# Performance work log

Measured on AMD Instinct MI355X. Metric: run time of the kernel, lower is better.

The kernel has to match this reference:

```python
import jax, jax.numpy as jnp
import numpy as np

S = 8192
D = 512

def setup_inputs() -> dict:
    key = jax.random.key(0)
    k1, k2, k3, k4 = jax.random.split(key, 4)
    token_encodings = jax.random.normal(k1, (S, D), dtype=jnp.float32)
    # causal mask: True where attention is disallowed (strictly upper triangular)
    mask = jnp.triu(jnp.ones((S, S), dtype=bool), k=1)
    W_q = jax.random.normal(k2, (D, D), dtype=jnp.float32) * (1.0 / np.sqrt(D))
    W_k = jax.random.normal(k3, (D, D), dtype=jnp.float32) * (1.0 / np.sqrt(D))
    W_v = jax.random.normal(k4, (D, D), dtype=jnp.float32) * (1.0 / np.sqrt(D))
    return {"token_encodings": token_encodings, "mask": mask, "W_q": W_q, "W_k": W_k, "W_v": W_v}

def reference(token_encodings, mask, W_q, W_k, W_v):
    # nn.Linear(bias=False): y = x @ W^T
    q = token_encodings @ W_q.T  # [S, D]
    k = token_encodings @ W_k.T  # [S, D]
    v = token_encodings @ W_v.T  # [S, D]
    scale = jnp.asarray(k.shape[1], dtype=q.dtype) ** 0.5
    sims = (q @ k.T) / scale  # [S, S]
    sims = jnp.where(mask, jnp.asarray(-1e9, dtype=sims.dtype), sims)
    attn = jax.nn.softmax(sims, axis=1)
    return attn @ v  # [S, D]
```

## Files before the change

### kernel.cpp

```cpp
#include <hip/hip_runtime.h>
#include <stdint.h>

typedef _Float16 f16;
typedef _Float16 f16x8 __attribute__((ext_vector_type(8)));
typedef _Float16 f16x4 __attribute__((ext_vector_type(4)));
typedef float f32x4 __attribute__((ext_vector_type(4)));

#define S_TOK 8192
#define DDIM  512
#define L2E   1.44269504088896340736f
#define QSCALE 0.04419417382415922f
#define NSLOT 320
#define GTOT  8320

__device__ __forceinline__ void gload_lds16(const void* g, void* l) {
  __builtin_amdgcn_global_load_lds((const __attribute__((address_space(1))) void*)g,
                                   (__attribute__((address_space(3))) void*)l, 16, 0, 0);
}

template <int C>
__device__ __forceinline__ float fdpp(float x) {
  return __builtin_bit_cast(float,
      __builtin_amdgcn_update_dpp(0, __builtin_bit_cast(int, x), C, 0xF, 0xF, true));
}
__device__ __forceinline__ float rowmax16(float x) {
  x = fmaxf(x, fdpp<0xB1>(x));
  x = fmaxf(x, fdpp<0x4E>(x));
  x = fmaxf(x, fdpp<0x141>(x));
  x = fmaxf(x, fdpp<0x140>(x));
  return x;
}
__device__ __forceinline__ float rowsum16(float x) {
  x += fdpp<0xB1>(x);
  x += fdpp<0x4E>(x);
  x += fdpp<0x141>(x);
  x += fdpp<0x140>(x);
  return x;
}

__global__ __launch_bounds__(256) void k_convert(
    const float* __restrict__ X, const float* __restrict__ Wq,
    const float* __restrict__ Wk, const float* __restrict__ Wv,
    f16* __restrict__ Xh, f16* __restrict__ Wh, int* __restrict__ tp) {
  const int SD = S_TOK * DDIM;
  const int DD = DDIM * DDIM;
  int gi = blockIdx.x * 256 + threadIdx.x;
  if (gi < NSLOT) tp[gi] = -1;
  int i4 = gi * 4;
  if (i4 < SD) {
    f32x4 v = *(const f32x4*)(X + i4);
    f16x4 h = {(f16)v[0], (f16)v[1], (f16)v[2], (f16)v[3]};
    *(f16x4*)(Xh + i4) = h;
  } else {
    int j = i4 - SD;
    int mat = j >> 18;
    const float* src = (mat == 0) ? Wq : (mat == 1 ? Wk : Wv);
    f32x4 v = *(const f32x4*)(src + (j & (DD - 1)));
    f16x4 h = {(f16)v[0], (f16)v[1], (f16)v[2], (f16)v[3]};
    *(f16x4*)(Wh + j) = h;
  }
}

__global__ __launch_bounds__(256) void k_proj(
    const f16* __restrict__ Xh, const f16* __restrict__ Wh,
    f16* __restrict__ Qh, f16* __restrict__ KB, f16* __restrict__ VB) {
  __shared__ __align__(16) char Al[128 * 128];
  __shared__ __align__(16) char Bl[128 * 128];
  const int tid = threadIdx.x;
  const int w = tid >> 6, lane = tid & 63;
  const int m0 = blockIdx.x * 128;
  const int n0 = blockIdx.y * 128;
  const int wr = (w >> 1) * 64;
  const int wc = (w & 1) * 64;

  f32x4 acc[4][4];
#pragma unroll
  for (int i = 0; i < 4; ++i)
#pragma unroll
    for (int j = 0; j < 4; ++j) acc[i][j] = (f32x4){0.f, 0.f, 0.f, 0.f};

  const char* Xb = (const char*)Xh;
  const char* Wb = (const char*)Wh;

  for (int kb = 0; kb < DDIM; kb += 64) {
    __syncthreads();
#pragma unroll
    for (int i = 0; i < 4; ++i) {
      int ch = w * 4 + i;
      int srow = lane >> 3;
      int scol = ((lane & 7) * 16) ^ (srow << 4);
      gload_lds16(Xb + (size_t)(m0 + ch * 8 + srow) * 1024 + kb * 2 + scol, Al + ch * 1024);
      gload_lds16(Wb + (size_t)(n0 + ch * 8 + srow) * 1024 + kb * 2 + scol, Bl + ch * 1024);
    }
    __syncthreads();
#pragma unroll
    for (int ks = 0; ks < 2; ++ks) {
      f16x8 a[4], b[4];
#pragma unroll
      for (int mf = 0; mf < 4; ++mf) {
        int row = wr + mf * 16 + (lane & 15);
        int col = (ks * 64 + ((lane >> 4) * 16)) ^ ((row & 7) << 4);
        a[mf] = *(const f16x8*)(Al + row * 128 + col);
      }
#pragma unroll
      for (int nf = 0; nf < 4; ++nf) {
        int row = wc + nf * 16 + (lane & 15);
        int col = (ks * 64 + ((lane >> 4) * 16)) ^ ((row & 7) << 4);
        b[nf] = *(const f16x8*)(Bl + row * 128 + col);
      }
#pragma unroll
      for (int mf = 0; mf < 4; ++mf)
#pragma unroll
        for (int nf = 0; nf < 4; ++nf)
          acc[mf][nf] = __builtin_amdgcn_mfma_f32_16x16x32_f16(a[mf], b[nf], acc[mf][nf], 0, 0, 0);
    }
  }
  int mat = n0 >> 9;
  int nbase = n0 & 511;
  if (mat == 2) {
#pragma unroll
    for (int mf = 0; mf < 4; ++mf) {
      int R0 = m0 + wr + mf * 16 + (lane >> 4) * 4;
      int K = R0 >> 5;
      int lhi = ((R0 >> 3) & 3) * 16;
      int j0 = R0 & 7;
#pragma unroll
      for (int nf = 0; nf < 4; ++nf) {
        int col = nbase + wc + nf * 16 + (lane & 15);
        f16x4 h = {(f16)acc[mf][nf][0], (f16)acc[mf][nf][1],
                   (f16)acc[mf][nf][2], (f16)acc[mf][nf][3]};
        *(f16x4*)((char*)VB + (size_t)(K * 32 + (col >> 4)) * 1024 +
                  (lhi + (col & 15)) * 16 + j0 * 2) = h;
      }
    }
  } else if (mat == 1) {
#pragma unroll
    for (int mf = 0; mf < 4; ++mf)
#pragma unroll
      for (int nf = 0; nf < 4; ++nf)
#pragma unroll
        for (int r = 0; r < 4; ++r) {
          int token = m0 + wr + mf * 16 + (lane >> 4) * 4 + r;
          int d = nbase + wc + nf * 16 + (lane & 15);
          size_t byte = (size_t)(token >> 5) * 32768 + (size_t)((token >> 4) & 1) * 16384
                      + (size_t)(d >> 5) * 1024
                      + (token & 15) * 16 + ((d >> 3) & 3) * 256 + (d & 7) * 2;
          *(f16*)((char*)KB + byte) = (f16)acc[mf][nf][r];
        }
  } else {
    float scale = QSCALE;
#pragma unroll
    for (int mf = 0; mf < 4; ++mf)
#pragma unroll
      for (int nf = 0; nf < 4; ++nf)
#pragma unroll
        for (int r = 0; r < 4; ++r) {
          int row = m0 + wr + mf * 16 + (lane >> 4) * 4 + r;
          int col = nbase + wc + nf * 16 + (lane & 15);
          Qh[(size_t)row * DDIM + col] = (f16)(acc[mf][nf][r] * scale);
        }
  }
}

__global__ __launch_bounds__(512, 2) void k_flash(
    const f16* __restrict__ Qh, const f16* __restrict__ KBg,
    const f16* __restrict__ VBg, f16* __restrict__ Opart,
    float* __restrict__ Mpart, float* __restrict__ Lpart,
    int* __restrict__ TilePart) {
  __shared__ __align__(16) char Kl[2][32768];
  __shared__ __align__(16) char Vl[2][32768];
  __shared__ __align__(16) char Pl[8][2][1152];

  const int tid = threadIdx.x;
  const int w = tid >> 6, lane = tid & 63;
  const int l15 = lane & 15, l4 = lane >> 4;

  int bid = blockIdx.x;
  int b = (bid & 7) * 32 + (bid >> 3);
  int g  = (GTOT * b) >> 8;
  int g1 = (GTOT * (b + 1)) >> 8;
  int t = 0;
  while (2 * (t + 1) * (t + 2) <= g) ++t;

  const char* Kb = (const char*)KBg;
  const char* Vb = (const char*)VBg;

#define STAGEKV(KB_, BI) do {                                                  \
    const char* ks_ = Kb + (size_t)((KB_) >> 5) * 32768;                       \
    _Pragma("unroll")                                                          \
    for (int i_ = 0; i_ < 4; ++i_) {                                           \
      int ch_ = w * 4 + i_;                                                    \
      gload_lds16(ks_ + ch_ * 1024 + lane * 16, Kl[BI] + ch_ * 1024);          \
    }                                                                          \
    const char* vs_ = Vb + (size_t)(KB_) * 1024;                               \
    _Pragma("unroll")                                                          \
    for (int i_ = 0; i_ < 4; ++i_) {                                           \
      int ch_ = w * 4 + i_;                                                    \
      gload_lds16(vs_ + ch_ * 1024 + lane * 16, Vl[BI] + ch_ * 1024);          \
    } } while (0)

#define SOFTMAX(KB_, Pdst) do {                                                \
    float p0[4], p1[4], mx[4];                                                 \
    int qrb = q0 + w * 16 + l4 * 4;                                            \
    int kc = (KB_) + l15;                                                      \
    _Pragma("unroll")                                                          \
    for (int r = 0; r < 4; ++r) {                                              \
      int qr = qrb + r;                                                        \
      float x0 = (kc      <= qr) ? s0[r] : -3.0e38f;                           \
      float x1 = (kc + 16 <= qr) ? s1[r] : -3.0e38f;                           \
      p0[r] = x0; p1[r] = x1;                                                  \
      mx[r] = rowmax16(fmaxf(x0, x1));                                         \
    }                                                                          \
    bool need = (mx[0] > mreg[0] + 8.f) || (mx[1] > mreg[1] + 8.f) ||          \
                (mx[2] > mreg[2] + 8.f) || (mx[3] > mreg[3] + 8.f);            \
    if (__any(need)) {                                                         \
      float alpha[4];                                                          \
      _Pragma("unroll")                                                        \
      for (int r = 0; r < 4; ++r) {                                            \
        float mn = fmaxf(mreg[r], mx[r]);                                      \
        alpha[r] = exp2f((mreg[r] - mn) * L2E);                                \
        lreg[r] *= alpha[r];                                                   \
        mreg[r] = mn;                                                          \
      }                                                                        \
      _Pragma("unroll")                                                        \
      for (int nf = 0; nf < 32; ++nf) {                                        \
        acc[nf][0] *= alpha[0];                                                \
        acc[nf][1] *= alpha[1];                                                \
        acc[nf][2] *= alpha[2];                                                \
        acc[nf][3] *= alpha[3];                                                \
      }                                                                        \
    }                                                                          \
    _Pragma("unroll")                                                          \
    for (int r = 0; r < 4; ++r) {                                              \
      int qr = qrb + r;                                                        \
      p0[r] = (kc      <= qr) ? exp2f((p0[r] - mreg[r]) * L2E) : 0.f;          \
      p1[r] = (kc + 16 <= qr) ? exp2f((p1[r] - mreg[r]) * L2E) : 0.f;          \
    }                                                                          \
    _Pragma("unroll")                                                          \
    for (int r = 0; r < 4; ++r) {                                              \
      int row = l4 * 4 + r;                                                    \
      *(f16*)((Pdst) + row * 72 + l15 * 2)      = (f16)p0[r];                  \
      *(f16*)((Pdst) + row * 72 + 32 + l15 * 2) = (f16)p1[r];                  \
    }                                                                          \
    _Pragma("unroll")                                                          \
    for (int r = 0; r < 4; ++r)                                                \
      lreg[r] += rowsum16(p0[r] + p1[r]);                                      \
  } while (0)

#define QKT(BUF) do {                                                          \
    s0 = (f32x4){0.f, 0.f, 0.f, 0.f};                                          \
    s1 = (f32x4){0.f, 0.f, 0.f, 0.f};                                          \
    const char* kp_ = (BUF) + lane * 16;                                       \
    __builtin_amdgcn_s_setprio(1);                                             \
    _Pragma("unroll")                                                          \
    for (int ks = 0; ks < 16; ++ks) {                                          \
      f16x8 kf0 = *(const f16x8*)(kp_ + ks * 1024);                            \
      s0 = __builtin_amdgcn_mfma_f32_16x16x32_f16(qf[ks], kf0, s0, 0, 0, 0);   \
      f16x8 kf1 = *(const f16x8*)(kp_ + 16384 + ks * 1024);                    \
      s1 = __builtin_amdgcn_mfma_f32_16x16x32_f16(qf[ks], kf1, s1, 0, 0, 0);   \
    }                                                                          \
    __builtin_amdgcn_s_setprio(0); } while (0)

#define PV(BI) do {                                                            \
    const char* VlB_ = Vl[BI] + lane * 16;                                     \
    const char* Pp_ = Pw + (BI) * 1152;                                        \
    f16x8 pa_ = *(const f16x8*)(Pp_ + l15 * 72 + l4 * 16);                     \
    __builtin_amdgcn_s_setprio(1);                                             \
    _Pragma("unroll")                                                          \
    for (int nf = 0; nf < 32; ++nf) {                                          \
      f16x8 vb_ = *(const f16x8*)(VlB_ + nf * 1024);                           \
      acc[nf] = __builtin_amdgcn_mfma_f32_16x16x32_f16(pa_, vb_, acc[nf], 0, 0, 0); \
    }                                                                          \
    __builtin_amdgcn_s_setprio(0); } while (0)

  char* Pw = (char*)Pl + (size_t)w * 2304;

  while (g < g1) {
    int Ct  = 2 * t * (t + 1);
    int Ct1 = 2 * (t + 1) * (t + 2);
    int gend = min(g1, Ct1);
    int n = gend - g;
    int kb0 = (g - Ct) * 32;
    int q0 = t * 128;
    int slot = b + t;

    f16x8 qf[16];
    {
      const f16* qp = Qh + (size_t)(q0 + w * 16 + l15) * DDIM + l4 * 8;
#pragma unroll
      for (int ks = 0; ks < 16; ++ks) qf[ks] = *(const f16x8*)(qp + ks * 32);
    }
    f32x4 acc[32];
#pragma unroll
    for (int i = 0; i < 32; ++i) acc[i] = (f32x4){0.f, 0.f, 0.f, 0.f};
    float mreg[4], lreg[4];
#pragma unroll
    for (int r = 0; r < 4; ++r) { mreg[r] = -3.0e38f; lreg[r] = 0.f; }
    f32x4 s0, s1;

    STAGEKV(kb0, 0);
    asm volatile("s_waitcnt vmcnt(0)" ::: "memory");
    __builtin_amdgcn_s_barrier();
    if (n > 1) STAGEKV(kb0 + 32, 1);
    QKT(Kl[0]);
    SOFTMAX(kb0, Pw);

    for (int it = 1; it < n; ++it) {
      PV((it - 1) & 1);
      asm volatile("s_waitcnt vmcnt(0)" ::: "memory");
      __builtin_amdgcn_s_barrier();
      if (it + 1 < n) STAGEKV(kb0 + (it + 1) * 32, (it + 1) & 1);
      QKT(Kl[it & 1]);
      SOFTMAX(kb0 + it * 32, Pw + (it & 1) * 1152);
    }

    PV((n - 1) & 1);
    __builtin_amdgcn_s_barrier();

    {
      float inv[4];
#pragma unroll
      for (int r = 0; r < 4; ++r) inv[r] = (lreg[r] > 0.f) ? 1.f / lreg[r] : 0.f;
      f16* op = Opart + (size_t)slot * (128 * 512);
      int rowb = w * 16 + l4 * 4;
#pragma unroll
      for (int nf = 0; nf < 32; ++nf) {
        int col = nf * 16 + l15;
#pragma unroll
        for (int r = 0; r < 4; ++r)
          op[(size_t)(rowb + r) * 512 + col] = (f16)(acc[nf][r] * inv[r]);
      }
      if (l15 == 0) {
#pragma unroll
        for (int r = 0; r < 4; ++r) {
          Mpart[slot * 128 + rowb + r] = mreg[r];
          Lpart[slot * 128 + rowb + r] = lreg[r];
        }
      }
      if (tid == 0) TilePart[slot] = t;
    }
    g = gend;
    ++t;
  }
#undef STAGEKV
#undef SOFTMAX
#undef QKT
#undef PV
}

__global__ __launch_bounds__(256) void k_reduce(
    const f16* __restrict__ Opart, const float* __restrict__ Mpart,
    const float* __restrict__ Lpart, const int* __restrict__ TilePart,
    float* __restrict__ out) {
  __shared__ int tp[NSLOT];
  __shared__ int sl[16];
  __shared__ int scnt;
  int tid = threadIdx.x;
  int t = blockIdx.x >> 2, rg = blockIdx.x & 3;
  for (int s = tid; s < NSLOT; s += 256) tp[s] = TilePart[s];
  __syncthreads();
  if (tid == 0) {
    int c = 0;
    for (int s = 0; s < NSLOT; ++s)
      if (tp[s] == t && c < 16) sl[c++] = s;
    scnt = c;
  }
  __syncthreads();
  int cnt = scnt;
  int rowIn = rg * 32 + (tid >> 3);
  int row = t * 128 + rowIn;
  int col0 = (tid & 7) * 64;

  float M = -3.0e38f;
  for (int i = 0; i < cnt; ++i) M = fmaxf(M, Mpart[sl[i] * 128 + rowIn]);
  float a[64];
#pragma unroll
  for (int j = 0; j < 64; ++j) a[j] = 0.f;
  float denom = 0.f;
  for (int i = 0; i < cnt; ++i) {
    int s = sl[i];
    float m = Mpart[s * 128 + rowIn];
    float l = Lpart[s * 128 + rowIn];
    float wgt = exp2f((m - M) * L2E) * l;
    denom += wgt;
    const f16* op = Opart + (size_t)s * 65536 + rowIn * 512 + col0;
#pragma unroll
    for (int v = 0; v < 8; ++v) {
      f16x8 x = *(const f16x8*)(op + v * 8);
#pragma unroll
      for (int j = 0; j < 8; ++j) a[v * 8 + j] += wgt * (float)x[j];
    }
  }
  float inv = (denom > 0.f) ? 1.f / denom : 0.f;
  float* o = out + (size_t)row * 512 + col0;
#pragma unroll
  for (int j = 0; j < 64; ++j) o[j] = a[j] * inv;
}

extern "C" void kernel_launch(void* const* d_in, const int* in_sizes, int n_in,
                              void* d_out, int out_size, void* d_ws, size_t ws_size,
                              hipStream_t stream) {
  const float* X  = (const float*)d_in[0];
  const float* Wq = (const float*)d_in[2];
  const float* Wk = (const float*)d_in[3];
  const float* Wv = (const float*)d_in[4];
  float* out = (float*)d_out;

  char* ws = (char*)d_ws;
  f16*   Opart = (f16*)(ws);
  float* Mpart = (float*)(ws + (40u << 20));
  float* Lpart = (float*)(ws + (41u << 20));
  int*   TileP = (int*)(ws + (42u << 20));
  f16* Qh = (f16*)(ws + (43u << 20));
  f16* KB = (f16*)(ws + (51u << 20));
  f16* VB = (f16*)(ws + (59u << 20));
  f16* Xh = (f16*)(ws + (67u << 20));
  f16* Wh = (f16*)(ws + (75u << 20));

  k_convert<<<4864, 256, 0, stream>>>(X, Wq, Wk, Wv, Xh, Wh, TileP);
  dim3 gp(64, 12);
  k_proj<<<gp, 256, 0, stream>>>(Xh, Wh, Qh, KB, VB);
  k_flash<<<256, 512, 0, stream>>>(Qh, KB, VB, Opart, Mpart, Lpart, TileP);
  k_reduce<<<256, 256, 0, stream>>>(Opart, Mpart, Lpart, TileP, out);
}
```

Before: 213.1 us.

## Repartition PV so each wave owns a 64-column output slice via shared P

```diff
diff --git a/kernel.cpp b/kernel.cpp
--- a/kernel.cpp
+++ b/kernel.cpp
@@ -5,6 +5,7 @@
 typedef _Float16 f16x8 __attribute__((ext_vector_type(8)));
 typedef _Float16 f16x4 __attribute__((ext_vector_type(4)));
 typedef float f32x4 __attribute__((ext_vector_type(4)));
+typedef int   i32x4 __attribute__((ext_vector_type(4)));
 
 #define S_TOK 8192
 #define DDIM  512
@@ -169,7 +170,10 @@
     int* __restrict__ TilePart) {
   __shared__ __align__(16) char Kl[2][32768];
   __shared__ __align__(16) char Vl[2][32768];
-  __shared__ __align__(16) char Pl[8][2][1152];
+  __shared__ __align__(16) char Pl[2][9216];
+  __shared__ __align__(16) float Alph[128];
+  __shared__ __align__(16) float Ll[128];
+  __shared__ __align__(16) int Fl[8];
 
   const int tid = threadIdx.x;
   const int w = tid >> 6, lane = tid & 63;
@@ -200,7 +204,7 @@
     } } while (0)
 
 #define SOFTMAX(KB_, Pdst) do {                                                \
-    float p0[4], p1[4], mx[4];                                                 \
+    float p0[4], p1[4], mx[4], alpha[4];                                       \
     int qrb = q0 + w * 16 + l4 * 4;                                            \
     int kc = (KB_) + l15;                                                      \
     _Pragma("unroll")                                                          \
@@ -213,8 +217,8 @@
     }                                                                          \
     bool need = (mx[0] > mreg[0] + 8.f) || (mx[1] > mreg[1] + 8.f) ||          \
                 (mx[2] > mreg[2] + 8.f) || (mx[3] > mreg[3] + 8.f);            \
-    if (__any(need)) {                                                         \
-      float alpha[4];                                                          \
+    need = __any(need);                                                        \
+    if (need) {                                                                \
       _Pragma("unroll")                                                        \
       for (int r = 0; r < 4; ++r) {                                            \
         float mn = fmaxf(mreg[r], mx[r]);                                      \
@@ -222,14 +226,15 @@
         lreg[r] *= alpha[r];                                                   \
         mreg[r] = mn;                                                          \
       }                                                                        \
+    } else {                                                                   \
       _Pragma("unroll")                                                        \
-      for (int nf = 0; nf < 32; ++nf) {                                        \
-        acc[nf][0] *= alpha[0];                                                \
-        acc[nf][1] *= alpha[1];                                                \
-        acc[nf][2] *= alpha[2];                                                \
-        acc[nf][3] *= alpha[3];                                                \
-      }                                                                        \
-    }                                                                          \
+      for (int r = 0; r < 4; ++r) alpha[r] = 1.0f;                             \
+    }                                                                          \
+    if (l15 == 0) {                                                            \
+      _Pragma("unroll")                                                        \
+      for (int r = 0; r < 4; ++r) Alph[w * 16 + l4 * 4 + r] = alpha[r];        \
+    }                                                                          \
+    if (lane == 0) Fl[w] = need ? 1 : 0;                                       \
     _Pragma("unroll")                                                          \
     for (int r = 0; r < 4; ++r) {                                              \
       int qr = qrb + r;                                                        \
@@ -238,7 +243,7 @@
     }                                                                          \
     _Pragma("unroll")                                                          \
     for (int r = 0; r < 4; ++r) {                                              \
-      int row = l4 * 4 + r;                                                    \
+      int row = w * 16 + l4 * 4 + r;                                           \
       *(f16*)((Pdst) + row * 72 + l15 * 2)      = (f16)p0[r];                  \
       *(f16*)((Pdst) + row * 72 + 32 + l15 * 2) = (f16)p1[r];                  \
     }                                                                          \
@@ -262,18 +267,36 @@
     __builtin_amdgcn_s_setprio(0); } while (0)
 
 #define PV(BI) do {                                                            \
-    const char* VlB_ = Vl[BI] + lane * 16;                                     \
-    const char* Pp_ = Pw + (BI) * 1152;                                        \
-    f16x8 pa_ = *(const f16x8*)(Pp_ + l15 * 72 + l4 * 16);                     \
+    i32x4 f0_ = *(const i32x4*)(Fl);                                           \
+    i32x4 f1_ = *(const i32x4*)(Fl + 4);                                       \
+    int fl_ = f0_[0] | f0_[1] | f0_[2] | f0_[3] | f1_[0] | f1_[1] | f1_[2] | f1_[3]; \
+    if (fl_) {                                                                 \
+      _Pragma("unroll")                                                        \
+      for (int rf = 0; rf < 8; ++rf) {                                         \
+        f32x4 av_ = *(const f32x4*)(Alph + rf * 16 + l4 * 4);                  \
+        _Pragma("unroll")                                                      \
+        for (int cf = 0; cf < 4; ++cf) {                                       \
+          acc[rf * 4 + cf][0] *= av_[0];                                       \
+          acc[rf * 4 + cf][1] *= av_[1];                                       \
+          acc[rf * 4 + cf][2] *= av_[2];                                       \
+          acc[rf * 4 + cf][3] *= av_[3];                                       \
+        }                                                                      \
+      }                                                                        \
+    }                                                                          \
+    f16x8 vbf_[4];                                                             \
+    _Pragma("unroll")                                                          \
+    for (int cf = 0; cf < 4; ++cf)                                             \
+      vbf_[cf] = *(const f16x8*)(Vl[BI] + (w * 4 + cf) * 1024 + lane * 16);    \
+    const char* pb_ = Pl[BI] + l15 * 72 + l4 * 16;                             \
     __builtin_amdgcn_s_setprio(1);                                             \
     _Pragma("unroll")                                                          \
-    for (int nf = 0; nf < 32; ++nf) {                                          \
-      f16x8 vb_ = *(const f16x8*)(VlB_ + nf * 1024);                           \
-      acc[nf] = __builtin_amdgcn_mfma_f32_16x16x32_f16(pa_, vb_, acc[nf], 0, 0, 0); \
+    for (int rf = 0; rf < 8; ++rf) {                                           \
+      f16x8 pa_ = *(const f16x8*)(pb_ + rf * 1152);                            \
+      _Pragma("unroll")                                                        \
+      for (int cf = 0; cf < 4; ++cf)                                           \
+        acc[rf * 4 + cf] = __builtin_amdgcn_mfma_f32_16x16x32_f16(pa_, vbf_[cf], acc[rf * 4 + cf], 0, 0, 0); \
     }                                                                          \
     __builtin_amdgcn_s_setprio(0); } while (0)
-
-  char* Pw = (char*)Pl + (size_t)w * 2304;
 
   while (g < g1) {
     int Ct  = 2 * t * (t + 1);
@@ -301,44 +324,54 @@
     STAGEKV(kb0, 0);
     asm volatile("s_waitcnt vmcnt(0)" ::: "memory");
     __builtin_amdgcn_s_barrier();
-    if (n > 1) STAGEKV(kb0 + 32, 1);
-    QKT(Kl[0]);
-    SOFTMAX(kb0, Pw);
-
-    for (int it = 1; it < n; ++it) {
-      PV((it - 1) & 1);
+
+    for (int it = 0; it < n; ++it) {
+      int cur = it & 1;
+      if (it + 1 < n) STAGEKV(kb0 + (it + 1) * 32, cur ^ 1);
+      QKT(Kl[cur]);
+      SOFTMAX(kb0 + it * 32, Pl[cur]);
+      asm volatile("s_waitcnt lgkmcnt(0)" ::: "memory");
+      __builtin_amdgcn_s_barrier();
+      PV(cur);
       asm volatile("s_waitcnt vmcnt(0)" ::: "memory");
       __builtin_amdgcn_s_barrier();
-      if (it + 1 < n) STAGEKV(kb0 + (it + 1) * 32, (it + 1) & 1);
-      QKT(Kl[it & 1]);
-      SOFTMAX(kb0 + it * 32, Pw + (it & 1) * 1152);
-    }
-
-    PV((n - 1) & 1);
+    }
+
+    if (l15 == 0) {
+#pragma unroll
+      for (int r = 0; r < 4; ++r) Ll[w * 16 + l4 * 4 + r] = lreg[r];
+    }
+    asm volatile("s_waitcnt lgkmcnt(0)" ::: "memory");
     __builtin_amdgcn_s_barrier();
-
     {
-      float inv[4];
-#pragma unroll
-      for (int r = 0; r < 4; ++r) inv[r] = (lreg[r] > 0.f) ? 1.f / lreg[r] : 0.f;
       f16* op = Opart + (size_t)slot * (128 * 512);
-      int rowb = w * 16 + l4 * 4;
-#pragma unroll
-      for (int nf = 0; nf < 32; ++nf) {
-        int col = nf * 16 + l15;
-#pragma unroll
-        for (int r = 0; r < 4; ++r)
-          op[(size_t)(rowb + r) * 512 + col] = (f16)(acc[nf][r] * inv[r]);
+#pragma unroll
+      for (int rf = 0; rf < 8; ++rf) {
+        f32x4 lv = *(const f32x4*)(Ll + rf * 16 + l4 * 4);
+        f32x4 inv;
+#pragma unroll
+        for (int r = 0; r < 4; ++r) inv[r] = (lv[r] > 0.f) ? 1.f / lv[r] : 0.f;
+#pragma unroll
+        for (int cf = 0; cf < 4; ++cf) {
+          int col = w * 64 + cf * 16 + l15;
+#pragma unroll
+          for (int r = 0; r < 4; ++r) {
+            int row = rf * 16 + l4 * 4 + r;
+            op[(size_t)row * 512 + col] = (f16)(acc[rf * 4 + cf][r] * inv[r]);
+          }
+        }
       }
       if (l15 == 0) {
 #pragma unroll
         for (int r = 0; r < 4; ++r) {
-          Mpart[slot * 128 + rowb + r] = mreg[r];
-          Lpart[slot * 128 + rowb + r] = lreg[r];
+          int row = w * 16 + l4 * 4 + r;
+          Mpart[slot * 128 + row] = mreg[r];
+          Lpart[slot * 128 + row] = lreg[r];
         }
       }
       if (tid == 0) TilePart[slot] = t;
     }
+    __builtin_amdgcn_s_barrier();
     g = gend;
     ++t;
   }
```

After: 286.6 us. +34.5%, slower.

## Fuse QK^T and PV MFMA loops and split K/V staging for overlap

Applied to the files above, without the earlier changes.

```diff
diff --git a/kernel.cpp b/kernel.cpp
--- a/kernel.cpp
+++ b/kernel.cpp
@@ -185,13 +185,15 @@
   const char* Kb = (const char*)KBg;
   const char* Vb = (const char*)VBg;
 
-#define STAGEKV(KB_, BI) do {                                                  \
+#define STAGEK(KB_, BI) do {                                                   \
     const char* ks_ = Kb + (size_t)((KB_) >> 5) * 32768;                       \
     _Pragma("unroll")                                                          \
     for (int i_ = 0; i_ < 4; ++i_) {                                           \
       int ch_ = w * 4 + i_;                                                    \
       gload_lds16(ks_ + ch_ * 1024 + lane * 16, Kl[BI] + ch_ * 1024);          \
-    }                                                                          \
+    } } while (0)
+
+#define STAGEV(KB_, BI) do {                                                   \
     const char* vs_ = Vb + (size_t)(KB_) * 1024;                               \
     _Pragma("unroll")                                                          \
     for (int i_ = 0; i_ < 4; ++i_) {                                           \
@@ -262,14 +264,35 @@
     __builtin_amdgcn_s_setprio(0); } while (0)
 
 #define PV(BI) do {                                                            \
-    const char* VlB_ = Vl[BI] + lane * 16;                                     \
+    const char* vp_ = Vl[BI] + lane * 16;                                      \
     const char* Pp_ = Pw + (BI) * 1152;                                        \
     f16x8 pa_ = *(const f16x8*)(Pp_ + l15 * 72 + l4 * 16);                     \
     __builtin_amdgcn_s_setprio(1);                                             \
     _Pragma("unroll")                                                          \
     for (int nf = 0; nf < 32; ++nf) {                                          \
-      f16x8 vb_ = *(const f16x8*)(VlB_ + nf * 1024);                           \
+      f16x8 vb_ = *(const f16x8*)(vp_ + nf * 1024);                            \
       acc[nf] = __builtin_amdgcn_mfma_f32_16x16x32_f16(pa_, vb_, acc[nf], 0, 0, 0); \
+    }                                                                          \
+    __builtin_amdgcn_s_setprio(0); } while (0)
+
+#define FUSED(KBUF, VBI) do {                                                  \
+    s0 = (f32x4){0.f, 0.f, 0.f, 0.f};                                          \
+    s1 = (f32x4){0.f, 0.f, 0.f, 0.f};                                          \
+    const char* kp_ = (KBUF) + lane * 16;                                      \
+    const char* vp_ = Vl[VBI] + lane * 16;                                     \
+    const char* Pp_ = Pw + (VBI) * 1152;                                       \
+    f16x8 pa_ = *(const f16x8*)(Pp_ + l15 * 72 + l4 * 16);                     \
+    __builtin_amdgcn_s_setprio(1);                                             \
+    _Pragma("unroll")                                                          \
+    for (int ks = 0; ks < 16; ++ks) {                                          \
+      f16x8 kf0 = *(const f16x8*)(kp_ + ks * 1024);                            \
+      s0 = __builtin_amdgcn_mfma_f32_16x16x32_f16(qf[ks], kf0, s0, 0, 0, 0);   \
+      f16x8 vb0 = *(const f16x8*)(vp_ + (2 * ks) * 1024);                      \
+      acc[2 * ks] = __builtin_amdgcn_mfma_f32_16x16x32_f16(pa_, vb0, acc[2 * ks], 0, 0, 0); \
+      f16x8 kf1 = *(const f16x8*)(kp_ + 16384 + ks * 1024);                    \
+      s1 = __builtin_amdgcn_mfma_f32_16x16x32_f16(qf[ks], kf1, s1, 0, 0, 0);   \
+      f16x8 vb1 = *(const f16x8*)(vp_ + (2 * ks + 1) * 1024);                  \
+      acc[2 * ks + 1] = __builtin_amdgcn_mfma_f32_16x16x32_f16(pa_, vb1, acc[2 * ks + 1], 0, 0, 0); \
     }                                                                          \
     __builtin_amdgcn_s_setprio(0); } while (0)
 
@@ -298,22 +321,29 @@
     for (int r = 0; r < 4; ++r) { mreg[r] = -3.0e38f; lreg[r] = 0.f; }
     f32x4 s0, s1;
 
-    STAGEKV(kb0, 0);
+    STAGEK(kb0, 0);
+    STAGEV(kb0, 0);
     asm volatile("s_waitcnt vmcnt(0)" ::: "memory");
     __builtin_amdgcn_s_barrier();
-    if (n > 1) STAGEKV(kb0 + 32, 1);
+    if (n > 1) STAGEK(kb0 + 32, 1);
     QKT(Kl[0]);
     SOFTMAX(kb0, Pw);
+    asm volatile("s_waitcnt lgkmcnt(0)" ::: "memory");
+    if (n > 1) STAGEV(kb0 + 32, 1);
 
     for (int it = 1; it < n; ++it) {
-      PV((it - 1) & 1);
-      asm volatile("s_waitcnt vmcnt(0)" ::: "memory");
+      asm volatile("s_waitcnt vmcnt(4)" ::: "memory");
       __builtin_amdgcn_s_barrier();
-      if (it + 1 < n) STAGEKV(kb0 + (it + 1) * 32, (it + 1) & 1);
-      QKT(Kl[it & 1]);
+      if (it + 1 < n) STAGEK(kb0 + (it + 1) * 32, (it + 1) & 1);
+      FUSED(Kl[it & 1], (it - 1) & 1);
+      __builtin_amdgcn_s_barrier();
+      if (it + 1 < n) STAGEV(kb0 + (it + 1) * 32, (it + 1) & 1);
       SOFTMAX(kb0 + it * 32, Pw + (it & 1) * 1152);
-    }
-
+      asm volatile("s_waitcnt lgkmcnt(0)" ::: "memory");
+    }
+
+    asm volatile("s_waitcnt vmcnt(0)" ::: "memory");
+    __builtin_amdgcn_s_barrier();
     PV((n - 1) & 1);
     __builtin_amdgcn_s_barrier();
 
@@ -342,10 +372,12 @@
     g = gend;
     ++t;
   }
-#undef STAGEKV
+#undef STAGEK
+#undef STAGEV
 #undef SOFTMAX
 #undef QKT
 #undef PV
+#undef FUSED
 }
 
 __global__ __launch_bounds__(256) void k_reduce(
```

After: 212.3 us. About the same (-0.3%).
